# Kernel tuning notes

Hardware: AMD Instinct MI355X
Metric: run time of the kernel (lower is better)

Reference implementation:

```python
import jax, jax.numpy as jnp
import numpy as np
from jax import lax

EPS = 1e-5

def _conv(x, w, b, stride, pad):
    y = lax.conv_general_dilated(x, w, (stride, stride), ((pad, pad), (pad, pad)),
                                 dimension_numbers=('NCHW', 'OIHW', 'NCHW'))
    return y + b[None, :, None, None]

def _deconv(x, w, b):
    # torch ConvTranspose2d(k=4, s=2, p=1): weight (Cin, Cout, 4, 4)
    w2 = jnp.flip(w, (2, 3)).transpose(1, 0, 2, 3)  # OIHW for forward conv
    y = lax.conv_general_dilated(x, w2, (1, 1), ((2, 2), (2, 2)),
                                 lhs_dilation=(2, 2),
                                 dimension_numbers=('NCHW', 'OIHW', 'NCHW'))
    return y + b[None, :, None, None]

def _bn(x, g, b):
    m = jnp.mean(x, axis=(0, 2, 3), keepdims=True)
    v = jnp.mean((x - m) ** 2, axis=(0, 2, 3), keepdims=True)
    return g[None, :, None, None] * (x - m) * lax.rsqrt(v + EPS) + b[None, :, None, None]

def setup_inputs() -> dict:
    key = jax.random.key(0)
    ks = jax.random.split(key, 16)
    f32 = jnp.float32
    def w(k, shape):
        return (jax.random.normal(k, shape, f32) * 0.05)
    inp = {
        'x': jax.random.uniform(ks[0], (32, 1, 512, 512), f32),
        'w1': w(ks[1], (16, 1, 4, 4)),  'b1': jnp.zeros((16,), f32), 'g1': jnp.ones((16,), f32), 'be1': jnp.zeros((16,), f32),
        'w2': w(ks[2], (16, 16, 4, 4)), 'b2': jnp.zeros((16,), f32), 'g2': jnp.ones((16,), f32), 'be2': jnp.zeros((16,), f32),
        'w3': w(ks[3], (4, 16, 4, 4)),  'b3': jnp.zeros((4,), f32),  'g3': jnp.ones((4,), f32),  'be3': jnp.zeros((4,), f32),
        'wpre': w(ks[4], (2, 4, 1, 1)), 'bpre': jnp.zeros((2,), f32),
        'codebook': w(ks[5], (256, 2)),
        'wpost': w(ks[6], (4, 2, 1, 1)), 'bpost': jnp.zeros((4,), f32),
        'wd1': w(ks[7], (4, 16, 4, 4)),  'bd1': jnp.zeros((16,), f32), 'g4': jnp.ones((16,), f32), 'be4': jnp.zeros((16,), f32),
        'wd2': w(ks[8], (16, 16, 4, 4)), 'bd2': jnp.zeros((16,), f32), 'g5': jnp.ones((16,), f32), 'be5': jnp.zeros((16,), f32),
        'wd3': w(ks[9], (16, 1, 4, 4)),  'bd3': jnp.zeros((1,), f32),
    }
    return inp

def _forward(x, w1, b1, g1, be1, w2, b2, g2, be2, w3, b3, g3, be3,
             wpre, bpre, codebook, wpost, bpost,
             wd1, bd1, g4, be4, wd2, bd2, g5, be5, wd3, bd3):
    # encoder: three stride-2 convs with BN + ReLU
    h = jax.nn.relu(_bn(_conv(x, w1, b1, 2, 1), g1, be1))
    h = jax.nn.relu(_bn(_conv(h, w2, b2, 2, 1), g2, be2))
    h = jax.nn.relu(_bn(_conv(h, w3, b3, 2, 1), g3, be3))
    q = _conv(h, wpre, bpre, 1, 0)          # [B, 2, H/8, W/8]
    B, C, Hq, Wq = q.shape
    qf = q.transpose(0, 2, 3, 1).reshape(B * Hq * Wq, C)   # [N, 2]
    # squared Euclidean distances to codebook (argmin equals cdist argmin)
    d2 = (jnp.sum(qf * qf, -1, keepdims=True)
          - 2.0 * qf @ codebook.T
          + jnp.sum(codebook * codebook, -1)[None, :])     # [N, 256]
    idx = jnp.argmin(d2, axis=-1)
    quant = codebook[idx]                                   # gather [N, 2]
    commitment_loss = jnp.mean((lax.stop_gradient(quant) - qf) ** 2)
    codebook_loss = jnp.mean((quant - lax.stop_gradient(qf)) ** 2)
    qout = qf + lax.stop_gradient(quant - qf)               # straight-through
    qout = qout.reshape(B, Hq, Wq, C).transpose(0, 3, 1, 2)
    d = _conv(qout, wpost, bpost, 1, 0)
    d = jax.nn.relu(_bn(_deconv(d, wd1, bd1), g4, be4))
    d = jax.nn.relu(_bn(_deconv(d, wd2, bd2), g5, be5))
    out = jax.nn.sigmoid(_deconv(d, wd3, bd3))
    recon = jnp.mean((x - out) ** 2)
    total = 1.0 * recon + codebook_loss + 0.2 * commitment_loss
    return out, total

def reference(x, w1, b1, g1, be1, w2, b2, g2, be2, w3, b3, g3, be3,
              wpre, bpre, codebook, wpost, bpost,
              wd1, bd1, g4, be4, wd2, bd2, g5, be5, wd3, bd3):
    return _forward(x, w1, b1, g1, be1, w2, b2, g2, be2, w3, b3, g3, be3,
                    wpre, bpre, codebook, wpost, bpost,
                    wd1, bd1, g4, be4, wd2, bd2, g5, be5, wd3, bd3)
```

## Files before the change

kernel.cpp:

```cpp
#include <hip/hip_runtime.h>
#include <hip/hip_bf16.h>
#include <math.h>

using bf16 = __hip_bfloat16;

__device__ __forceinline__ float b2f(bf16 v) { return __bfloat162float(v); }
__device__ __forceinline__ float ldv(const void* p, size_t i, int m) {
  return m ? b2f(((const bf16*)p)[i]) : ((const float*)p)[i];
}

struct D2 { double s, s2; };

__device__ __forceinline__ void block_stats1(float v, D2* slot) {
  float v2 = v * v;
#pragma unroll
  for (int o = 32; o; o >>= 1) { v += __shfl_down(v, o, 64); v2 += __shfl_down(v2, o, 64); }
  __shared__ float a1[4], a2[4];
  int lane = threadIdx.x & 63, w = threadIdx.x >> 6;
  if (lane == 0) { a1[w] = v; a2[w] = v2; }
  __syncthreads();
  if (threadIdx.x == 0) {
    slot->s  = (double)a1[0] + a1[1] + a1[2] + a1[3];
    slot->s2 = (double)a2[0] + a2[1] + a2[2] + a2[3];
  }
}

__device__ __forceinline__ void block_stats1d(double v, double v2, D2* slot) {
#pragma unroll
  for (int o = 32; o; o >>= 1) { v += __shfl_down(v, o, 64); v2 += __shfl_down(v2, o, 64); }
  __shared__ double q1[4], q2[4];
  int lane = threadIdx.x & 63, w = threadIdx.x >> 6;
  if (lane == 0) { q1[w] = v; q2[w] = v2; }
  __syncthreads();
  if (threadIdx.x == 0) { slot->s = q1[0] + q1[1] + q1[2] + q1[3]; slot->s2 = q2[0] + q2[1] + q2[2] + q2[3]; }
}

__device__ __forceinline__ void block_sum1(float v, double* slot) {
#pragma unroll
  for (int o = 32; o; o >>= 1) v += __shfl_down(v, o, 64);
  __shared__ float a1[4];
  int lane = threadIdx.x & 63, w = threadIdx.x >> 6;
  if (lane == 0) a1[w] = v;
  __syncthreads();
  if (threadIdx.x == 0) *slot = (double)a1[0] + a1[1] + a1[2] + a1[3];
}

__device__ __forceinline__ void block_stats16(const float* vs, const float* vq, D2* base, int NB, int bx) {
  __shared__ float s1[64], s2[64];
  int lane = threadIdx.x & 63, w = threadIdx.x >> 6;
#pragma unroll
  for (int co = 0; co < 16; co++) {
    float v = vs[co], v2 = vq[co];
#pragma unroll
    for (int o = 32; o; o >>= 1) { v += __shfl_down(v, o, 64); v2 += __shfl_down(v2, o, 64); }
    if (lane == 0) { s1[co * 4 + w] = v; s2[co * 4 + w] = v2; }
  }
  __syncthreads();
  if (threadIdx.x < 16) {
    int co = threadIdx.x;
    base[co * NB + bx].s  = (double)s1[co * 4] + s1[co * 4 + 1] + s1[co * 4 + 2] + s1[co * 4 + 3];
    base[co * NB + bx].s2 = (double)s2[co * 4] + s2[co * 4 + 1] + s2[co * 4 + 2] + s2[co * 4 + 3];
  }
}

__global__ void init_k(const unsigned* __restrict__ xw, int* flag) {
  unsigned lo = xw[threadIdx.x] & 0xFFFFu;
  int inr = (lo >= 0x3000u && lo < 0x4000u) ? 1 : 0;
  unsigned long long b = __ballot(inr);
  __shared__ int cnt[4];
  if ((threadIdx.x & 63) == 0) cnt[threadIdx.x >> 6] = __popcll(b);
  __syncthreads();
  if (threadIdx.x == 0) *flag = (cnt[0] + cnt[1] + cnt[2] + cnt[3] >= 128) ? 1 : 0;
}

__global__ void prep_k(const void* w1, const void* b1, const void* w2, const void* b2,
                       const void* w3, const void* b3, const void* wpre, const void* bpre,
                       const void* cbk, const void* wpost, const void* bpost,
                       const void* wd1, const void* bd1, const void* wd2, const void* bd2,
                       const void* wd3, const void* bd3,
                       const void* g1, const void* be1, const void* g2, const void* be2,
                       const void* g3, const void* be3, const void* g4, const void* be4,
                       const void* g5, const void* be5,
                       float* __restrict__ PF, double* __restrict__ PD, const int* modep) {
  int m = *modep, t = threadIdx.x;
  for (int i = t; i < 256; i += 256) PF[i] = ldv(w1, i, m);
  if (t < 16) PF[256 + t] = ldv(b1, t, m);
  for (int i = t; i < 4096; i += 256) PF[272 + i] = ldv(w2, i, m);
  if (t < 16) PF[4368 + t] = ldv(b2, t, m);
  for (int i = t; i < 1024; i += 256) {
    int co = i >> 6, ci = (i >> 4) & 3, tap = i & 15;
    PF[4384 + i] = ldv(wd1, ci * 256 + co * 16 + tap, m);
  }
  if (t < 16) PF[5408 + t] = ldv(bd1, t, m);
  for (int i = t; i < 4096; i += 256) {
    int co = i >> 8, ci = (i >> 4) & 15, tap = i & 15;
    PF[5424 + i] = ldv(wd2, ci * 256 + co * 16 + tap, m);
  }
  for (int i = t; i < 4096; i += 256) {
    int ci = i >> 8, tap = (i >> 4) & 15, co = i & 15;
    PF[10272 + i] = ldv(wd2, ci * 256 + co * 16 + tap, m);
  }
  if (t < 16) PF[9520 + t] = ldv(bd2, t, m);
  for (int i = t; i < 256; i += 256) PF[9536 + i] = ldv(wd3, i, m);
  {
    int tap = t >> 4, ci = t & 15;
    PF[10016 + t] = ldv(wd3, ci * 16 + tap, m);
  }
  if (t == 0) PF[9792] = ldv(bd3, 0, m);
  if (t < 16) {
    PF[9856 + t] = ldv(g1, t, m);  PF[9872 + t] = ldv(be1, t, m);
    PF[9888 + t] = ldv(g2, t, m);  PF[9904 + t] = ldv(be2, t, m);
    PF[9952 + t] = ldv(g4, t, m);  PF[9968 + t] = ldv(be4, t, m);
    PF[9984 + t] = ldv(g5, t, m);  PF[10000 + t] = ldv(be5, t, m);
  }
  if (t < 4) { PF[9920 + t] = ldv(g3, t, m); PF[9936 + t] = ldv(be3, t, m); }
  for (int i = t; i < 1024; i += 256) PD[i] = ldv(w3, i, m);
  if (t < 4) PD[1024 + t] = ldv(b3, t, m);
  if (t < 8) PD[1028 + t] = ldv(wpre, t, m);
  if (t < 2) PD[1036 + t] = ldv(bpre, t, m);
  for (int i = t; i < 512; i += 256) PD[1040 + i] = ldv(cbk, i, m);
  if (t < 8) PD[1552 + t] = ldv(wpost, t, m);
  if (t < 4) PD[1560 + t] = ldv(bpost, t, m);
}

__global__ __launch_bounds__(256) void bn_reduce_k(const D2* __restrict__ part, int NB,
                                                   double* __restrict__ stD, float* __restrict__ stF,
                                                   const float* __restrict__ gb, double invN) {
  int c = blockIdx.x;
  double s = 0, s2 = 0;
  for (int i = threadIdx.x; i < NB; i += 256) { D2 p = part[c * NB + i]; s += p.s; s2 += p.s2; }
#pragma unroll
  for (int o = 32; o; o >>= 1) { s += __shfl_down(s, o, 64); s2 += __shfl_down(s2, o, 64); }
  __shared__ double l1[4], l2[4];
  int lane = threadIdx.x & 63, w = threadIdx.x >> 6;
  if (lane == 0) { l1[w] = s; l2[w] = s2; }
  __syncthreads();
  if (threadIdx.x == 0) {
    double S = l1[0] + l1[1] + l1[2] + l1[3], Q = l2[0] + l2[1] + l2[2] + l2[3];
    double mu = S * invN, var = Q * invN - mu * mu;
    if (var < 0) var = 0;
    double sc = (double)gb[c] / sqrt(var + 1e-5);
    double sh = (double)gb[16 + c] - mu * sc;
    stD[c] = sc; stD[16 + c] = sh;
    stF[c] = (float)sc; stF[16 + c] = (float)sh;
  }
}

__global__ __launch_bounds__(256) void conv1_t(const void* __restrict__ x, const float* __restrict__ PF,
                                               float* __restrict__ y, D2* __restrict__ part,
                                               const int* modep) {
  const int m = *modep;
  __shared__ float sx[10 * 130];
  int t = threadIdx.x;
  int bx = blockIdx.x;
  int b = bx >> 8, r = bx & 255, tY = r >> 2, tX = r & 3;
  int iy0 = 8 * tY - 1, ix0 = 128 * tX - 1;
  size_t xb = (size_t)b * 262144;
  for (int i = t; i < 1300; i += 256) {
    int ry = i / 130, rx = i - ry * 130;
    int gy = iy0 + ry, gx = ix0 + rx;
    float v = 0.f;
    if ((unsigned)gy < 512u && (unsigned)gx < 512u) v = ldv(x, xb + (size_t)gy * 512 + gx, m);
    sx[i] = v;
  }
  __syncthreads();
  int tyy = t >> 6, txx = t & 63;
  int oy = tY * 4 + tyy, ox = tX * 64 + txx;
  float acc[16];
#pragma unroll
  for (int co = 0; co < 16; co++) acc[co] = PF[256 + co];
  int ly = 2 * tyy, lx = 2 * txx;
#pragma unroll
  for (int ky = 0; ky < 4; ky++) {
#pragma unroll
    for (int kx = 0; kx < 4; kx++) {
      float v = sx[(ly + ky) * 130 + lx + kx];
#pragma unroll
      for (int co = 0; co < 16; co++) acc[co] = fmaf(v, PF[co * 16 + ky * 4 + kx], acc[co]);
    }
  }
  int rem = oy * 256 + ox;
  float vq_[16];
#pragma unroll
  for (int co = 0; co < 16; co++) {
    y[((size_t)(b * 16 + co) << 16) + rem] = acc[co];
    vq_[co] = acc[co] * acc[co];
  }
  block_stats16(acc, vq_, part, 8192, bx);
}

__global__ __launch_bounds__(256) void conv2_t(const float* __restrict__ h1, const float* __restrict__ PF,
                                               const float* __restrict__ aff, float* __restrict__ h2,
                                               D2* __restrict__ part) {
  __shared__ float su[34 * 34];
  int t = threadIdx.x, ty = t >> 4, tx = t & 15;
  int bx = blockIdx.x, bb = bx >> 6, r = bx & 63, tY = r >> 3, tX = r & 7;
  int oy = tY * 16 + ty, ox = tX * 16 + tx;
  int iy0 = 32 * tY - 1, ix0 = 32 * tX - 1;
  const float* W2 = PF + 272;
  float acc[16];
#pragma unroll
  for (int co = 0; co < 16; co++) acc[co] = PF[4368 + co];
  for (int ci = 0; ci < 16; ci++) {
    __syncthreads();
    float sc = aff[ci], sh = aff[16 + ci];
    const float* ib = h1 + ((size_t)(bb * 16 + ci) << 16);
    for (int i = t; i < 1156; i += 256) {
      int riy = i / 34, rix = i - riy * 34;
      int gy = iy0 + riy, gx = ix0 + rix;
      float v = 0.f;
      if ((unsigned)gy < 256u && (unsigned)gx < 256u) v = fmaxf(fmaf(ib[gy * 256 + gx], sc, sh), 0.f);
      su[i] = v;
    }
    __syncthreads();
    const float* wci = W2 + ci * 16;
#pragma unroll
    for (int ky = 0; ky < 4; ky++) {
#pragma unroll
      for (int kx = 0; kx < 4; kx++) {
        float v = su[(2 * ty + ky) * 34 + 2 * tx + kx];
        const float* wt = wci + ky * 4 + kx;
#pragma unroll
        for (int co = 0; co < 16; co++) acc[co] = fmaf(v, wt[co * 256], acc[co]);
      }
    }
  }
  float vq_[16];
#pragma unroll
  for (int co = 0; co < 16; co++) {
    h2[((size_t)(bb * 16 + co) * 128 + oy) * 128 + ox] = acc[co];
    vq_[co] = acc[co] * acc[co];
  }
  block_stats16(acc, vq_, part, 2048, bx);
}

__global__ __launch_bounds__(256) void conv3_k(const float* __restrict__ h2, const double* __restrict__ PD,
                                               const float* __restrict__ aff, double* __restrict__ c3,
                                               D2* __restrict__ part) {
  const int co = blockIdx.y;
  int idx = blockIdx.x * 256 + threadIdx.x;
  int b = idx >> 12, rem = idx & 4095, oy = rem >> 6, ox = rem & 63;
  double acc = PD[1024 + co];
  int iy0 = 2 * oy - 1, ix0 = 2 * ox - 1;
  for (int ci = 0; ci < 16; ci++) {
    const float* ib = h2 + (size_t)(b * 16 + ci) * 16384;
    float sc = aff[ci], sh = aff[16 + ci];
    const double* wr = PD + co * 256 + ci * 16;
#pragma unroll
    for (int ky = 0; ky < 4; ky++) {
      int iy = iy0 + ky;
      if ((unsigned)iy < 128u) {
        const float* row = ib + iy * 128;
#pragma unroll
        for (int kx = 0; kx < 4; kx++) {
          int ix = ix0 + kx;
          if ((unsigned)ix < 128u) {
            float v = fmaxf(fmaf(row[ix], sc, sh), 0.f);
            acc = fma((double)v, wr[ky * 4 + kx], acc);
          }
        }
      }
    }
  }
  c3[(size_t)(b * 4 + co) * 4096 + rem] = acc;
  block_stats1d(acc, acc * acc, part + (co * 512 + blockIdx.x));
}

__global__ __launch_bounds__(256) void vq_k(const double* __restrict__ c3, const double* __restrict__ PD,
                                            const double* __restrict__ stD2, float* __restrict__ d0,
                                            double* __restrict__ vp) {
  __shared__ double cb[512];
  for (int i = threadIdx.x; i < 512; i += 256) cb[i] = PD[1040 + i];
  __syncthreads();
  int pix = blockIdx.x * 256 + threadIdx.x;
  int b = pix >> 12, rem = pix & 4095;
  const double* hb = c3 + (size_t)b * 16384 + rem;
  double q0 = PD[1036], q1 = PD[1037];
#pragma unroll
  for (int ci = 0; ci < 4; ci++) {
    double v = fma(hb[ci * 4096], stD2[ci], stD2[16 + ci]);
    if (v < 0) v = 0;
    q0 = fma(v, PD[1028 + ci], q0);
    q1 = fma(v, PD[1032 + ci], q1);
  }
  int best = 0;
  double bd = 1e300;
  for (int k = 0; k < 256; k++) {
    double dx = q0 - cb[2 * k], dy = q1 - cb[2 * k + 1];
    double d = dx * dx + dy * dy;
    if (d < bd) { bd = d; best = k; }
  }
  double c0 = cb[2 * best], c1 = cb[2 * best + 1];
  double e0 = q0 - c0, e1 = q1 - c1;
  float* ob = d0 + (size_t)b * 16384 + rem;
#pragma unroll
  for (int c = 0; c < 4; c++)
    ob[c * 4096] = (float)(PD[1560 + c] + PD[1552 + 2 * c] * c0 + PD[1552 + 2 * c + 1] * c1);
  double v = e0 * e0 + e1 * e1;
#pragma unroll
  for (int o = 32; o; o >>= 1) v += __shfl_down(v, o, 64);
  __shared__ double l1[4];
  int lane = threadIdx.x & 63, w = threadIdx.x >> 6;
  if (lane == 0) l1[w] = v;
  __syncthreads();
  if (threadIdx.x == 0) vp[blockIdx.x] = l1[0] + l1[1] + l1[2] + l1[3];
}

__global__ __launch_bounds__(256) void deconv1_k(const float* __restrict__ d0, const float* __restrict__ PF,
                                                 float* __restrict__ d1, D2* __restrict__ part) {
  const int co = blockIdx.y;
  __shared__ float wl[64];
  if (threadIdx.x < 64) wl[threadIdx.x] = PF[4384 + co * 64 + threadIdx.x];
  __syncthreads();
  int idx = blockIdx.x * 256 + threadIdx.x;
  int b = idx >> 14, rem = idx & 16383, oy = rem >> 7, ox = rem & 127;
  float acc = PF[5408 + co];
  int ry = (oy + 1) & 1, rx = (ox + 1) & 1;
#pragma unroll
  for (int ci = 0; ci < 4; ci++) {
    const float* ib = d0 + (size_t)(b * 4 + ci) * 4096;
    const float* wr = wl + ci * 16;
#pragma unroll
    for (int t2y = 0; t2y < 2; t2y++) {
      int ky = ry + 2 * t2y, iy = (oy + 1 - ky) >> 1;
      if ((unsigned)iy < 64u) {
#pragma unroll
        for (int t2x = 0; t2x < 2; t2x++) {
          int kx = rx + 2 * t2x, ix = (ox + 1 - kx) >> 1;
          if ((unsigned)ix < 64u) acc = fmaf(ib[iy * 64 + ix], wr[ky * 4 + kx], acc);
        }
      }
    }
  }
  d1[(size_t)(b * 16 + co) * 16384 + rem] = acc;
  block_stats1(acc, part + (co * 2048 + blockIdx.x));
}

__global__ __launch_bounds__(256) void deconv2_t(const float* __restrict__ d1, const float* __restrict__ PF,
                                                 const float* __restrict__ aff, float* __restrict__ d2,
                                                 D2* __restrict__ part) {
  __shared__ float su[16 * 324];
  int t = threadIdx.x, py = t >> 4, px = t & 15;
  int bx = blockIdx.x, bb = bx >> 6, r = bx & 63, tY = r >> 3, tX = r & 7;
  int iy0 = 16 * tY - 1, ix0 = 16 * tX - 1;
  for (int i = t; i < 5184; i += 256) {
    int ci = i / 324, rr = i - ci * 324;
    int riy = rr / 18, rix = rr - riy * 18;
    int gy = iy0 + riy, gx = ix0 + rix;
    float v = 0.f;
    if ((unsigned)gy < 128u && (unsigned)gx < 128u)
      v = fmaxf(fmaf(d1[(size_t)(bb * 16 + ci) * 16384 + gy * 128 + gx], aff[ci], aff[16 + ci]), 0.f);
    su[i] = v;
  }
  __syncthreads();
  const float* WT = PF + 10272;
  float vs[16], vq[16];
#pragma unroll
  for (int co = 0; co < 16; co++) { vs[co] = 0.f; vq[co] = 0.f; }
#pragma unroll
  for (int a = 0; a < 2; a++) {
#pragma unroll
    for (int bc = 0; bc < 2; bc++) {
      float acc[16];
#pragma unroll
      for (int co = 0; co < 16; co++) acc[co] = PF[9520 + co];
      int base = (py + a) * 18 + (px + bc);
      for (int ci = 0; ci < 16; ci++) {
        const float* sb = su + ci * 324 + base;
        float v00 = sb[0], v01 = sb[1], v10 = sb[18], v11 = sb[19];
        const float* wci = WT + ci * 256;
        const float* w00p = wci + (((3 - a) * 4 + (3 - bc)) << 4);
        const float* w01p = wci + (((3 - a) * 4 + (1 - bc)) << 4);
        const float* w10p = wci + (((1 - a) * 4 + (3 - bc)) << 4);
        const float* w11p = wci + (((1 - a) * 4 + (1 - bc)) << 4);
#pragma unroll
        for (int co = 0; co < 16; co++) {
          float s0 = fmaf(v00, w00p[co], acc[co]);
          float s1 = fmaf(v01, w01p[co], s0);
          float s2 = fmaf(v10, w10p[co], s1);
          acc[co] = fmaf(v11, w11p[co], s2);
        }
      }
      int oy = 32 * tY + 2 * py + a, ox = 32 * tX + 2 * px + bc;
      float4* dst = (float4*)(d2 + ((size_t)bb * 65536 + (size_t)oy * 256 + ox) * 16);
      dst[0] = make_float4(acc[0],  acc[1],  acc[2],  acc[3]);
      dst[1] = make_float4(acc[4],  acc[5],  acc[6],  acc[7]);
      dst[2] = make_float4(acc[8],  acc[9],  acc[10], acc[11]);
      dst[3] = make_float4(acc[12], acc[13], acc[14], acc[15]);
#pragma unroll
      for (int co = 0; co < 16; co++) {
        vs[co] += acc[co];
        vq[co] = fmaf(acc[co], acc[co], vq[co]);
      }
    }
  }
  block_stats16(vs, vq, part, 2048, bx);
}

__device__ __forceinline__ int swz(int p, int g) {
  int s = p * 4 + (g ^ (p & 3));
  return s ^ (((p >> 2) & 1) << 2);
}

__device__ __forceinline__ float4 aff_relu(float4 v, float4 sc, float4 sh) {
  v.x = fmaxf(fmaf(v.x, sc.x, sh.x), 0.f);
  v.y = fmaxf(fmaf(v.y, sc.y, sh.y), 0.f);
  v.z = fmaxf(fmaf(v.z, sc.z, sh.z), 0.f);
  v.w = fmaxf(fmaf(v.w, sc.w, sh.w), 0.f);
  return v;
}

__device__ __forceinline__ void dot4(float& a, float4 v, float4 w) {
  a = fmaf(v.x, w.x, a); a = fmaf(v.y, w.y, a);
  a = fmaf(v.z, w.z, a); a = fmaf(v.w, w.w, a);
}

__global__ __launch_bounds__(256, 4) void deconv3_t(const float* __restrict__ d2, const float* __restrict__ PF,
                                                    const float* __restrict__ aff, const void* __restrict__ x,
                                                    void* __restrict__ outp, double* __restrict__ rp,
                                                    const int* __restrict__ modep) {
  const int m = *modep;
  __shared__ float4 sd4[1296];
  int t = threadIdx.x;
  int bx = blockIdx.x;
  int b = bx >> 8, r = bx & 255, tY = r >> 4, tX = r & 15;
  int iy0 = 16 * tY - 1, ix0 = 16 * tX - 1;
  const float4* A4 = (const float4*)aff;
  float4 SC0 = A4[0], SC1 = A4[1], SC2 = A4[2], SC3 = A4[3];
  float4 SH0 = A4[4], SH1 = A4[5], SH2 = A4[6], SH3 = A4[7];
  const float* db = d2 + (size_t)b * 1048576;
  for (int p = t; p < 324; p += 256) {
    int riy = p / 18, rix = p - riy * 18;
    int gy = iy0 + riy, gx = ix0 + rix;
    float4 v0, v1, v2, v3;
    if ((unsigned)gy < 256u && (unsigned)gx < 256u) {
      const float4* s = (const float4*)(db + ((size_t)gy * 256 + gx) * 16);
      v0 = aff_relu(s[0], SC0, SH0);
      v1 = aff_relu(s[1], SC1, SH1);
      v2 = aff_relu(s[2], SC2, SH2);
      v3 = aff_relu(s[3], SC3, SH3);
    } else {
      v0 = v1 = v2 = v3 = make_float4(0.f, 0.f, 0.f, 0.f);
    }
    sd4[swz(p, 0)] = v0; sd4[swz(p, 1)] = v1; sd4[swz(p, 2)] = v2; sd4[swz(p, 3)] = v3;
  }
  __syncthreads();

  int lx = t & 15, ly = t >> 4;
  float bias = PF[9792];
  float a00 = bias, a01 = bias, a10 = bias, a11 = bias;
  const float* WT = PF + 10016;
  int p00 = ly * 18 + lx;
#define TAPW(ky, kx) (*(const float4*)(WT + ((ky) * 4 + (kx)) * 16 + (g << 2)))
#pragma unroll
  for (int g = 0; g < 4; g++) {
    float4 w33 = TAPW(3, 3), w31 = TAPW(3, 1), w32 = TAPW(3, 2), w30 = TAPW(3, 0);
    float4 w13 = TAPW(1, 3), w11 = TAPW(1, 1), w12 = TAPW(1, 2), w10 = TAPW(1, 0);
    float4 w23 = TAPW(2, 3), w21 = TAPW(2, 1), w22 = TAPW(2, 2), w20 = TAPW(2, 0);
    float4 w03 = TAPW(0, 3), w01 = TAPW(0, 1), w02 = TAPW(0, 2), w00 = TAPW(0, 0);
    float4 v;
    v = sd4[swz(p00, g)];      dot4(a00, v, w33);
    v = sd4[swz(p00 + 1, g)];  dot4(a00, v, w31); dot4(a01, v, w32);
    v = sd4[swz(p00 + 2, g)];  dot4(a01, v, w30);
    v = sd4[swz(p00 + 18, g)]; dot4(a00, v, w13); dot4(a10, v, w23);
    v = sd4[swz(p00 + 19, g)]; dot4(a00, v, w11); dot4(a01, v, w12); dot4(a10, v, w21); dot4(a11, v, w22);
    v = sd4[swz(p00 + 20, g)]; dot4(a01, v, w10); dot4(a11, v, w20);
    v = sd4[swz(p00 + 36, g)]; dot4(a10, v, w03);
    v = sd4[swz(p00 + 37, g)]; dot4(a10, v, w01); dot4(a11, v, w02);
    v = sd4[swz(p00 + 38, g)]; dot4(a11, v, w00);
  }
#undef TAPW

  int oy = 32 * tY + 2 * ly, ox = 32 * tX + 2 * lx;
  size_t ob = (size_t)b * 262144 + (size_t)oy * 512 + ox;
  float o0 = 1.f / (1.f + expf(-a00));
  float o1 = 1.f / (1.f + expf(-a01));
  float o2 = 1.f / (1.f + expf(-a10));
  float o3 = 1.f / (1.f + expf(-a11));
  if (m) {
    bf16* op = (bf16*)outp;
    op[ob] = __float2bfloat16(o0);       op[ob + 1] = __float2bfloat16(o1);
    op[ob + 512] = __float2bfloat16(o2); op[ob + 513] = __float2bfloat16(o3);
  } else {
    float* op = (float*)outp;
    op[ob] = o0;       op[ob + 1] = o1;
    op[ob + 512] = o2; op[ob + 513] = o3;
  }
  float d0_ = ldv(x, ob, m) - o0;
  float d1_ = ldv(x, ob + 1, m) - o1;
  float d2_ = ldv(x, ob + 512, m) - o2;
  float d3_ = ldv(x, ob + 513, m) - o3;
  float ds = fmaf(d0_, d0_, fmaf(d1_, d1_, fmaf(d2_, d2_, d3_ * d3_)));
  block_sum1(ds, rp + bx);
}

__global__ __launch_bounds__(256) void finalize_k(const double* __restrict__ vp, const double* __restrict__ rp,
                                                  void* outp, const int* modep) {
  double s = 0, rr = 0;
  for (int i = threadIdx.x; i < 512; i += 256) s += vp[i];
  for (int i = threadIdx.x; i < 8192; i += 256) rr += rp[i];
#pragma unroll
  for (int o = 32; o; o >>= 1) { s += __shfl_down(s, o, 64); rr += __shfl_down(rr, o, 64); }
  __shared__ double l1[4], l2[4];
  int lane = threadIdx.x & 63, w = threadIdx.x >> 6;
  if (lane == 0) { l1[w] = s; l2[w] = rr; }
  __syncthreads();
  if (threadIdx.x == 0) {
    double S = l1[0] + l1[1] + l1[2] + l1[3], R = l2[0] + l2[1] + l2[2] + l2[3];
    double total = R * (1.0 / 8388608.0) + 1.2 * (S * (1.0 / 262144.0));
    if (*modep) ((bf16*)outp)[8388608] = __float2bfloat16((float)total);
    else        ((float*)outp)[8388608] = (float)total;
  }
}

extern "C" void kernel_launch(void* const* d_in, const int* in_sizes, int n_in,
                              void* d_out, int out_size, void* d_ws, size_t ws_size,
                              hipStream_t stream) {
  const void* x    = d_in[0];
  const void* w1   = d_in[1];  const void* b1  = d_in[2];
  const void* g1   = d_in[3];  const void* be1 = d_in[4];
  const void* w2   = d_in[5];  const void* b2  = d_in[6];
  const void* g2   = d_in[7];  const void* be2 = d_in[8];
  const void* w3   = d_in[9];  const void* b3  = d_in[10];
  const void* g3   = d_in[11]; const void* be3 = d_in[12];
  const void* wpre = d_in[13]; const void* bpre= d_in[14];
  const void* cbk  = d_in[15];
  const void* wpost= d_in[16]; const void* bpost= d_in[17];
  const void* wd1  = d_in[18]; const void* bd1 = d_in[19];
  const void* g4   = d_in[20]; const void* be4 = d_in[21];
  const void* wd2  = d_in[22]; const void* bd2 = d_in[23];
  const void* g5   = d_in[24]; const void* be5 = d_in[25];
  const void* wd3  = d_in[26]; const void* bd3 = d_in[27];

  char* ws = (char*)d_ws;
  int*    MODE = (int*)ws;
  float*  STF  = (float*)(ws + 1024);
  double* STD  = (double*)(ws + 4096);
  float*  PF   = (float*)(ws + 8192);
  double* PD   = (double*)(ws + 73728);
  D2*     P1   = (D2*)(ws + 131072);
  D2*     P2   = (D2*)(ws + 2228224);
  D2*     P3   = (D2*)(ws + 2752512);
  D2*     P4   = (D2*)(ws + 2785280);
  D2*     P5   = (D2*)(ws + 3309568);
  double* VP   = (double*)(ws + 3833856);
  double* RP   = (double*)(ws + 3837952);
  char* HB = ws + 6291456;
  float*  H1  = (float*)HB;
  float*  H2  = (float*)(HB + 134217728);
  double* C3  = (double*)HB;
  float*  D0  = (float*)(HB + 165675008);
  float*  D1  = (float*)HB;
  float*  D2T = (float*)(HB + 33554432);

  init_k<<<1, 256, 0, stream>>>((const unsigned*)x, MODE);
  prep_k<<<1, 256, 0, stream>>>(w1, b1, w2, b2, w3, b3, wpre, bpre, cbk, wpost, bpost,
                                wd1, bd1, wd2, bd2, wd3, bd3,
                                g1, be1, g2, be2, g3, be3, g4, be4, g5, be5, PF, PD, MODE);

  conv1_t<<<8192, 256, 0, stream>>>(x, PF, H1, P1, MODE);
  bn_reduce_k<<<16, 256, 0, stream>>>(P1, 8192, STD + 0, STF + 0, PF + 9856, 1.0 / 2097152.0);

  conv2_t<<<2048, 256, 0, stream>>>(H1, PF, STF + 0, H2, P2);
  bn_reduce_k<<<16, 256, 0, stream>>>(P2, 2048, STD + 32, STF + 32, PF + 9888, 1.0 / 524288.0);

  conv3_k<<<dim3(512, 4), 256, 0, stream>>>(H2, PD, STF + 32, C3, P3);
  bn_reduce_k<<<4, 256, 0, stream>>>(P3, 512, STD + 64, STF + 64, PF + 9920, 1.0 / 131072.0);

  vq_k<<<512, 256, 0, stream>>>(C3, PD, STD + 64, D0, VP);

  deconv1_k<<<dim3(2048, 16), 256, 0, stream>>>(D0, PF, D1, P4);
  bn_reduce_k<<<16, 256, 0, stream>>>(P4, 2048, STD + 96, STF + 96, PF + 9952, 1.0 / 524288.0);

  deconv2_t<<<2048, 256, 0, stream>>>(D1, PF, STF + 96, D2T, P5);
  bn_reduce_k<<<16, 256, 0, stream>>>(P5, 2048, STD + 128, STF + 128, PF + 9984, 1.0 / 2097152.0);

  deconv3_t<<<8192, 256, 0, stream>>>(D2T, PF, STF + 128, x, d_out, RP, MODE);
  finalize_k<<<1, 256, 0, stream>>>(VP, RP, d_out, MODE);
}
```

Before: 636.9 us.

## Store conv1 output channel-last and load four channels per pass in conv2

Conv1 now writes its 16-channel output in NHWC order with float4 stores instead of 16 strided planar stores. Conv2 reads four channels at a time as float4, processing 4 channel groups per tile instead of 16 single-channel passes. It keeps even and odd columns in separate shared-memory planes to avoid stride-2 bank conflicts. The conv2 weights are repacked to match, and launch bounds ask for 8 blocks per CU. The larger shared tile could limit occupancy, and any other consumer of h1 must also expect the new layout.

```diff
diff --git a/kernel.cpp b/kernel.cpp
--- a/kernel.cpp
+++ b/kernel.cpp
@@ -85,7 +85,10 @@
   int m = *modep, t = threadIdx.x;
   for (int i = t; i < 256; i += 256) PF[i] = ldv(w1, i, m);
   if (t < 16) PF[256 + t] = ldv(b1, t, m);
-  for (int i = t; i < 4096; i += 256) PF[272 + i] = ldv(w2, i, m);
+  for (int i = t; i < 4096; i += 256) {
+    int cig = i >> 10, tap = (i >> 6) & 15, c4 = (i >> 4) & 3, co = i & 15;
+    PF[272 + i] = ldv(w2, co * 256 + (cig * 4 + c4) * 16 + tap, m);
+  }
   if (t < 16) PF[4368 + t] = ldv(b2, t, m);
   for (int i = t; i < 1024; i += 256) {
     int co = i >> 6, ci = (i >> 4) & 3, tap = i & 15;
@@ -180,48 +183,69 @@
     }
   }
   int rem = oy * 256 + ox;
+  float4* dst = (float4*)(y + ((size_t)b * 65536 + rem) * 16);
+  dst[0] = make_float4(acc[0],  acc[1],  acc[2],  acc[3]);
+  dst[1] = make_float4(acc[4],  acc[5],  acc[6],  acc[7]);
+  dst[2] = make_float4(acc[8],  acc[9],  acc[10], acc[11]);
+  dst[3] = make_float4(acc[12], acc[13], acc[14], acc[15]);
   float vq_[16];
 #pragma unroll
-  for (int co = 0; co < 16; co++) {
-    y[((size_t)(b * 16 + co) << 16) + rem] = acc[co];
-    vq_[co] = acc[co] * acc[co];
-  }
+  for (int co = 0; co < 16; co++) vq_[co] = acc[co] * acc[co];
   block_stats16(acc, vq_, part, 8192, bx);
 }
 
-__global__ __launch_bounds__(256) void conv2_t(const float* __restrict__ h1, const float* __restrict__ PF,
-                                               const float* __restrict__ aff, float* __restrict__ h2,
-                                               D2* __restrict__ part) {
-  __shared__ float su[34 * 34];
+__device__ __forceinline__ float4 aff_relu4(float4 v, float4 sc, float4 sh) {
+  v.x = fmaxf(fmaf(v.x, sc.x, sh.x), 0.f);
+  v.y = fmaxf(fmaf(v.y, sc.y, sh.y), 0.f);
+  v.z = fmaxf(fmaf(v.z, sc.z, sh.z), 0.f);
+  v.w = fmaxf(fmaf(v.w, sc.w, sh.w), 0.f);
+  return v;
+}
+
+__global__ __launch_bounds__(256, 8) void conv2_t(const float* __restrict__ h1, const float* __restrict__ PF,
+                                                  const float* __restrict__ aff, float* __restrict__ h2,
+                                                  D2* __restrict__ part) {
+  __shared__ float su[4896];
   int t = threadIdx.x, ty = t >> 4, tx = t & 15;
   int bx = blockIdx.x, bb = bx >> 6, r = bx & 63, tY = r >> 3, tX = r & 7;
   int oy = tY * 16 + ty, ox = tX * 16 + tx;
   int iy0 = 32 * tY - 1, ix0 = 32 * tX - 1;
   const float* W2 = PF + 272;
+  const float4* A4 = (const float4*)aff;
+  const float* hb = h1 + (size_t)bb * 1048576;
   float acc[16];
 #pragma unroll
   for (int co = 0; co < 16; co++) acc[co] = PF[4368 + co];
-  for (int ci = 0; ci < 16; ci++) {
+#pragma unroll
+  for (int g = 0; g < 4; g++) {
     __syncthreads();
-    float sc = aff[ci], sh = aff[16 + ci];
-    const float* ib = h1 + ((size_t)(bb * 16 + ci) << 16);
+    float4 SC = A4[g], SH = A4[4 + g];
     for (int i = t; i < 1156; i += 256) {
       int riy = i / 34, rix = i - riy * 34;
       int gy = iy0 + riy, gx = ix0 + rix;
-      float v = 0.f;
-      if ((unsigned)gy < 256u && (unsigned)gx < 256u) v = fmaxf(fmaf(ib[gy * 256 + gx], sc, sh), 0.f);
-      su[i] = v;
+      float4 v = make_float4(0.f, 0.f, 0.f, 0.f);
+      if ((unsigned)gy < 256u && (unsigned)gx < 256u)
+        v = aff_relu4(*(const float4*)(hb + ((size_t)gy * 256 + gx) * 16 + g * 4), SC, SH);
+      int s = (rix & 1) * 2448 + riy * 18 + (rix >> 1);
+      su[s] = v.x; su[612 + s] = v.y; su[1224 + s] = v.z; su[1836 + s] = v.w;
     }
     __syncthreads();
-    const float* wci = W2 + ci * 16;
+    const float* wg = W2 + g * 1024;
+    int base = 2 * ty * 18 + tx;
 #pragma unroll
     for (int ky = 0; ky < 4; ky++) {
 #pragma unroll
       for (int kx = 0; kx < 4; kx++) {
-        float v = su[(2 * ty + ky) * 34 + 2 * tx + kx];
-        const float* wt = wci + ky * 4 + kx;
-#pragma unroll
-        for (int co = 0; co < 16; co++) acc[co] = fmaf(v, wt[co * 256], acc[co]);
+        int s = (kx & 1) * 2448 + ky * 18 + (kx >> 1) + base;
+        float v0 = su[s], v1 = su[612 + s], v2 = su[1224 + s], v3 = su[1836 + s];
+        const float* wt = wg + (ky * 4 + kx) * 64;
+#pragma unroll
+        for (int co = 0; co < 16; co++) {
+          float s0 = fmaf(v0, wt[co], acc[co]);
+          float s1 = fmaf(v1, wt[16 + co], s0);
+          float s2 = fmaf(v2, wt[32 + co], s1);
+          acc[co] = fmaf(v3, wt[48 + co], s2);
+        }
       }
     }
   }
```

Result: faster. 617.2 us (-3.1%).
